# Optimization experiments

Measured on AMD Instinct MI355X. Metric: run time of the kernel, lower is better.

Reference implementation:

```python
import jax, jax.numpy as jnp
import numpy as np
import math

SEQ = 16384      # total ragged tokens
DIM = 1280       # vision hidden size
HEADS = 16
HDIM = DIM // HEADS  # 80
NSEG = 16        # number of segments (images); equal lengths of 1024


def rotate_half(x):
    x1, x2 = jnp.split(x, 2, axis=-1)
    return jnp.concatenate([-x2, x1], axis=-1)


def setup_inputs() -> dict:
    key = jax.random.key(0)
    ks = jax.random.split(key, 6)
    hidden_states = jax.random.normal(ks[0], (SEQ, DIM), dtype=jnp.float32)
    # rotary tables over the full head_dim (Qwen vision style: freqs duplicated)
    inv_freq = 1.0 / (10000.0 ** (jnp.arange(0, HDIM, 2, dtype=jnp.float32) / HDIM))
    pos = jnp.arange(SEQ, dtype=jnp.float32)
    freqs = jnp.outer(pos, inv_freq)                      # [S, HDIM/2]
    emb = jnp.concatenate([freqs, freqs], axis=-1)        # [S, HDIM]
    cos, sin = jnp.cos(emb), jnp.sin(emb)
    w_qkv = jax.random.normal(ks[1], (3 * DIM, DIM), dtype=jnp.float32) * 0.02
    b_qkv = jax.random.normal(ks[2], (3 * DIM,), dtype=jnp.float32) * 0.02
    w_proj = jax.random.normal(ks[3], (DIM, DIM), dtype=jnp.float32) * 0.02
    b_proj = jax.random.normal(ks[4], (DIM,), dtype=jnp.float32) * 0.02
    cu_seqlens = jnp.arange(NSEG + 1, dtype=jnp.int32) * (SEQ // NSEG)
    return {"hidden_states": hidden_states, "cos": cos, "sin": sin,
            "w_qkv": w_qkv, "b_qkv": b_qkv, "w_proj": w_proj, "b_proj": b_proj,
            "cu_seqlens": cu_seqlens}


def reference(hidden_states, cos, sin, w_qkv, b_qkv, w_proj, b_proj, cu_seqlens):
    S, D = hidden_states.shape
    hd = cos.shape[-1]
    nh = D // hd
    nseg = cu_seqlens.shape[0] - 1
    L = S // nseg  # equal segment lengths (matches cu_seqlens built in setup)

    qkv = hidden_states @ w_qkv.T + b_qkv                 # [S, 3D]
    qkv = qkv.reshape(S, 3, nh, hd)
    q, k, v = qkv[:, 0], qkv[:, 1], qkv[:, 2]             # [S, H, hd]

    # rotary (computed in float32, as in the original)
    c = cos[:, None, :]
    s = sin[:, None, :]
    q = q * c + rotate_half(q) * s
    k = k * c + rotate_half(k) * s

    # block-diagonal attention: reshape ragged-equal segments into a batch dim
    qs = q.reshape(nseg, L, nh, hd)
    ks = k.reshape(nseg, L, nh, hd)
    vs = v.reshape(nseg, L, nh, hd)

    scale = 1.0 / math.sqrt(hd)
    scores = jnp.einsum('bqhd,bkhd->bhqk', qs, ks) * scale   # [nseg, H, L, L]
    probs = jax.nn.softmax(scores, axis=-1)
    out = jnp.einsum('bhqk,bkhd->bqhd', probs, vs)           # [nseg, L, H, hd]
    out = out.reshape(S, D)
    return out @ w_proj.T + b_proj
```

## Files before the change

### kernel.cpp

```cpp
#include <hip/hip_runtime.h>

#define SEQ 16384
#define DIM 1280
#define NH 16
#define HD 80
#define NSEG 16
#define SEGL 1024

typedef __attribute__((ext_vector_type(8))) short bf16x8;
typedef __attribute__((ext_vector_type(4))) float f32x4;

__device__ inline unsigned short f2bf(float f){
  unsigned int x = __builtin_bit_cast(unsigned int, f);
  unsigned int r = (x + 0x7FFFu + ((x >> 16) & 1u)) >> 16;
  return (unsigned short)r;
}
__device__ inline float bf2f(unsigned short u){
  unsigned int x = ((unsigned int)u) << 16;
  return __builtin_bit_cast(float, x);
}
__device__ inline int cvtpk_bf16(float lo, float hi){
  int r;
  asm("v_cvt_pk_bf16_f32 %0, %1, %2" : "=v"(r) : "v"(lo), "v"(hi));
  return r;
}

__device__ inline void gload16(const unsigned short* g, unsigned short* l){
  __builtin_amdgcn_global_load_lds((const __attribute__((address_space(1))) void*)g,
                                   (__attribute__((address_space(3))) void*)l, 16, 0, 0);
}

__global__ __launch_bounds__(256) void pack3_kernel(const float* __restrict__ a,
    const float* __restrict__ b, const float* __restrict__ c,
    unsigned short* __restrict__ da, unsigned short* __restrict__ db,
    unsigned short* __restrict__ dc, int na, int nb){
  int i = blockIdx.x * 256 + threadIdx.x;
  const float* s; unsigned short* d; int j;
  if (i < na){ s = a; d = da; j = i; }
  else if (i < na + nb){ s = b; d = db; j = i - na; }
  else { s = c; d = dc; j = i - na - nb; }
  float4 v = ((const float4*)s)[j];
  ushort4 o;
  o.x = f2bf(v.x); o.y = f2bf(v.y); o.z = f2bf(v.z); o.w = f2bf(v.w);
  ((ushort4*)d)[j] = o;
}

template<int EPI>
__global__ __launch_bounds__(512, 2) void gemm256_kernel(const unsigned short* __restrict__ A,
    const unsigned short* __restrict__ B, const float* __restrict__ bias,
    void* __restrict__ Cout, unsigned short* __restrict__ Vtg, int M, int N, int K){
  __shared__ __attribute__((aligned(16))) unsigned short As[2][16384];
  __shared__ __attribute__((aligned(16))) unsigned short Bs[2][16384];
  const int nwg = gridDim.x;
  int bid = blockIdx.x;
  int swz = (bid & 7) * (nwg >> 3) + (bid >> 3);
  const int ntn = N >> 8;
  const int tm = (swz / ntn) << 8;
  const int tn = (swz % ntn) << 8;
  const int tid = threadIdx.x;
  const int wid = tid >> 6, l = tid & 63;
  const int lr = l & 15, lh = l >> 4;
  const int wrM = (wid >> 2) << 7;
  const int wcN = (wid & 3) << 6;
  const int NITER = K >> 7;

  const int srow = wid*8 + (l >> 3);
  const int scol = ((l & 7) ^ (l >> 3)) << 3;
  const int sldsu = wid << 9;

  const unsigned short* Ag = A + (size_t)tm * K;
  const unsigned short* Bg = B + (size_t)tn * K;

  const int ck0 = (lh*8) ^ ((l & 7) << 3);
  const int ck1 = (32 + lh*8) ^ ((l & 7) << 3);
  const int raA = (wrM + lr) << 6;
  const int raB = (wcN + lr) << 6;

  f32x4 zf = {0.f,0.f,0.f,0.f};
  f32x4 acc[8][4];
  #pragma unroll
  for (int i=0;i<8;i++)
    #pragma unroll
    for (int j=0;j<4;j++) acc[i][j] = zf;

#define STAGE_A(tile, h, q) gload16(Ag + (size_t)((h)*128 + (q)*64 + srow)*K + ((tile)<<6) + scol, \
                                    &As[(tile)&1][(h)*8192 + (q)*4096 + sldsu])
#define STAGE_B(tile, h, q) gload16(Bg + (size_t)((h)*128 + (q)*64 + srow)*K + ((tile)<<6) + scol, \
                                    &Bs[(tile)&1][(h)*8192 + (q)*4096 + sldsu])
#define RD_A(b, MOFF) \
  _Pragma("unroll") \
  for (int mi=0; mi<4; ++mi){ \
    a[0][mi] = *(const bf16x8*)&As[b][raA + ((MOFF)+mi)*1024 + ck0]; \
    a[1][mi] = *(const bf16x8*)&As[b][raA + ((MOFF)+mi)*1024 + ck1]; }
#define RD_B(b, NOFF, BREG) \
  _Pragma("unroll") \
  for (int nj=0; nj<2; ++nj){ \
    BREG[0][nj] = *(const bf16x8*)&Bs[b][raB + ((NOFF)+nj)*1024 + ck0]; \
    BREG[1][nj] = *(const bf16x8*)&Bs[b][raB + ((NOFF)+nj)*1024 + ck1]; }
#define BAR() __builtin_amdgcn_s_barrier();
#define QMFMA(MB, NB, BREG) \
  __builtin_amdgcn_s_setprio(1); \
  _Pragma("unroll") \
  for (int mi=0; mi<4; ++mi){ \
    _Pragma("unroll") \
    for (int nj=0; nj<2; ++nj){ \
      acc[(MB)+mi][(NB)+nj] = __builtin_amdgcn_mfma_f32_16x16x32_bf16(a[0][mi], BREG[0][nj], acc[(MB)+mi][(NB)+nj], 0,0,0); \
      acc[(MB)+mi][(NB)+nj] = __builtin_amdgcn_mfma_f32_16x16x32_bf16(a[1][mi], BREG[1][nj], acc[(MB)+mi][(NB)+nj], 0,0,0); \
    } \
  } \
  __builtin_amdgcn_s_setprio(0); \
  __builtin_amdgcn_s_barrier();

  #pragma unroll
  for (int q=0;q<2;q++){ STAGE_A(0,0,q); }
  #pragma unroll
  for (int q=0;q<2;q++){ STAGE_A(0,1,q); }
  #pragma unroll
  for (int q=0;q<2;q++){ STAGE_B(0,0,q); }
  #pragma unroll
  for (int q=0;q<2;q++){ STAGE_B(0,1,q); }
  #pragma unroll
  for (int q=0;q<2;q++){ STAGE_B(1,0,q); }
  #pragma unroll
  for (int q=0;q<2;q++){ STAGE_B(1,1,q); }
  #pragma unroll
  for (int q=0;q<2;q++){ STAGE_A(1,0,q); }
  #pragma unroll
  for (int q=0;q<2;q++){ STAGE_A(1,1,q); }
  asm volatile("s_waitcnt vmcnt(8)" ::: "memory");
  __builtin_amdgcn_s_barrier();

  for (int i=0; i<NITER; ++i){
    const int T = 2*i;
    const bool st = (i+1 < NITER);
    bf16x8 a[2][4], bx[2][2], by[2][2];

    RD_B(0, 0, bx); RD_A(0, 0);
    BAR(); QMFMA(0, 0, bx);

    RD_B(0, 2, by);
    BAR(); QMFMA(0, 2, by);

    RD_A(0, 4);
    if (st){ STAGE_B(T+2, 0, 0); STAGE_B(T+2, 0, 1); }
    BAR(); QMFMA(4, 2, by);

    if (st){
      STAGE_B(T+2, 1, 0); STAGE_B(T+2, 1, 1);
      STAGE_A(T+2, 0, 0); STAGE_A(T+2, 0, 1);
      asm volatile("s_waitcnt vmcnt(6)" ::: "memory");
    } else {
      asm volatile("s_waitcnt vmcnt(0)" ::: "memory");
    }
    BAR(); QMFMA(4, 0, bx);

    RD_B(1, 0, bx); RD_A(1, 0);
    if (st){ STAGE_A(T+2, 1, 0); STAGE_A(T+2, 1, 1); }
    BAR(); QMFMA(0, 0, bx);

    RD_B(1, 2, by);
    BAR(); QMFMA(0, 2, by);

    RD_A(1, 4);
    if (st){ STAGE_B(T+3, 0, 0); STAGE_B(T+3, 0, 1); STAGE_B(T+3, 1, 0); STAGE_B(T+3, 1, 1); }
    BAR(); QMFMA(4, 2, by);

    if (st){
      STAGE_A(T+3, 0, 0); STAGE_A(T+3, 0, 1); STAGE_A(T+3, 1, 0); STAGE_A(T+3, 1, 1);
      asm volatile("s_waitcnt vmcnt(8)" ::: "memory");
    }
    BAR(); QMFMA(4, 0, bx);
  }

#undef STAGE_A
#undef STAGE_B
#undef RD_A
#undef RD_B
#undef BAR
#undef QMFMA

  #pragma unroll
  for (int nj=0;nj<4;nj++){
    int col = tn + wcN + nj*16 + lr;
    float bv = bias[col];
    if (EPI == 0){
      int which = col / DIM;
      int rem = col - which*DIM;
      int hh = rem / HD;
      int d = rem - hh*HD;
      if (which == 2){
        unsigned short* Vd = Vtg + ((size_t)hh * HD + d) * SEQ;
        #pragma unroll
        for (int mi=0;mi<8;mi++){
          int row0 = tm + wrM + mi*16 + lh*4;
          int g = (row0 >> 2) & 15;
          int pg = ((g>>3)<<3) + ((g&3)<<1) + ((g>>2)&1);
          int s = (row0 & ~63) + pg*4;
          unsigned int w0 = (unsigned int)cvtpk_bf16(acc[mi][nj][0]+bv, acc[mi][nj][1]+bv);
          unsigned int w1 = (unsigned int)cvtpk_bf16(acc[mi][nj][2]+bv, acc[mi][nj][3]+bv);
          uint2 ov = {w0, w1};
          *(uint2*)(Vd + s) = ov;
        }
      } else {
        unsigned short* Q = (unsigned short*)Cout;
        size_t base = (size_t)(which*NH + hh) * SEQ;
        #pragma unroll
        for (int mi=0;mi<8;mi++){
          #pragma unroll
          for (int r=0;r<4;r++){
            int row = tm + wrM + mi*16 + lh*4 + r;
            Q[(base + row)*HD + d] = f2bf(acc[mi][nj][r] + bv);
          }
        }
      }
    } else {
      float* C = (float*)Cout;
      #pragma unroll
      for (int mi=0;mi<8;mi++){
        #pragma unroll
        for (int r=0;r<4;r++){
          int row = tm + wrM + mi*16 + lh*4 + r;
          C[(size_t)row*N + col] = acc[mi][nj][r] + bv;
        }
      }
    }
  }
}

__global__ __launch_bounds__(256) void rope_kernel(unsigned short* __restrict__ QKV,
    const float* __restrict__ cosb, const float* __restrict__ sinb){
  unsigned int gid = blockIdx.x * 256 + threadIdx.x;
  int pc = gid % 5;
  unsigned int row = gid / 5;
  int s = row % SEQ;
  int pd = pc * 8;
  float f = (row < (unsigned)(NH*SEQ)) ? (0.111803398874989485f * 1.4426950408889634f) : 1.0f;
  unsigned short* p = QKV + (size_t)row * HD;
  union { uint4 u4; unsigned short h[8]; } x1, x2, y1, y2;
  x1.u4 = *(const uint4*)(p + pd);
  x2.u4 = *(const uint4*)(p + pd + 40);
  float4 c0 = *(const float4*)(cosb + s*HD + pd);
  float4 c1 = *(const float4*)(cosb + s*HD + pd + 4);
  float4 s0 = *(const float4*)(sinb + s*HD + pd);
  float4 s1 = *(const float4*)(sinb + s*HD + pd + 4);
  float cc[8] = {c0.x,c0.y,c0.z,c0.w,c1.x,c1.y,c1.z,c1.w};
  float ss[8] = {s0.x,s0.y,s0.z,s0.w,s1.x,s1.y,s1.z,s1.w};
  #pragma unroll
  for (int j=0;j<8;j++){
    float a = bf2f(x1.h[j]), b = bf2f(x2.h[j]);
    y1.h[j] = f2bf((a*cc[j] - b*ss[j])*f);
    y2.h[j] = f2bf((b*cc[j] + a*ss[j])*f);
  }
  *(uint4*)(p + pd)      = y1.u4;
  *(uint4*)(p + pd + 40) = y2.u4;
}

__global__ __launch_bounds__(512) void attn_kernel(const unsigned short* __restrict__ QKV,
                                                   const unsigned short* __restrict__ Vt,
                                                   unsigned short* __restrict__ AO){
  int bid = blockIdx.x;
  int qt  = (bid >> 3) & 7;
  int g   = (bid & 7) * 32 + (bid >> 6);
  int h   = g & 15;
  int seg = g >> 4;
  int tid = threadIdx.x, wid = tid >> 6, l = tid & 63;
  int lr = l & 15, lh = l >> 4;
  const unsigned short* Qb = QKV + (size_t)(0*NH + h) * SEQ * HD;
  const unsigned short* Kb = QKV + (size_t)(1*NH + h) * SEQ * HD;
  const unsigned short* Vtb = Vt + (size_t)h * HD * SEQ;
  int q0 = seg*SEGL + qt*128;
  __shared__ __attribute__((aligned(16))) unsigned short Ksm[10240];
  __shared__ __attribute__((aligned(16))) unsigned short Vtsm[10240];
  bf16x8 qf[3];
  {
    const unsigned short* qp = Qb + (size_t)(q0 + wid*16 + lr) * HD;
    #pragma unroll
    for (int c=0;c<3;c++){
      int d0 = c*32 + lh*8;
      bf16x8 z = {0,0,0,0,0,0,0,0};
      qf[c] = (d0 < HD) ? *(const bf16x8*)(qp + d0) : z;
    }
  }
  f32x4 zf = {0.f,0.f,0.f,0.f};
  f32x4 o[5];
  #pragma unroll
  for (int dt=0;dt<5;dt++) o[dt] = zf;
  f32x4 lsumv = zf;
  float m = -1e30f;
  for (int kt=0; kt<8; kt++){
    int k0 = seg*SEGL + kt*128;
    const unsigned short* Ksrc = Kb + (size_t)k0 * HD;
    gload16(Ksrc + (wid*64 + l)*8,        &Ksm[wid*512]);
    gload16(Ksrc + (512 + wid*64 + l)*8,  &Ksm[4096 + wid*512]);
    if (wid < 4){
      gload16(Ksrc + (1024 + wid*64 + l)*8, &Ksm[8192 + wid*512]);
    } else {
      int cv = (wid-4)*64 + l;
      int d = cv >> 4, c16 = cv & 15;
      gload16(Vtb + (size_t)d*SEQ + k0 + ((c16 ^ (d & 15)) << 3), &Vtsm[(wid-4)*512]);
    }
    { int cv = 256 + wid*64 + l;
      int d = cv >> 4, c16 = cv & 15;
      gload16(Vtb + (size_t)d*SEQ + k0 + ((c16 ^ (d & 15)) << 3), &Vtsm[2048 + wid*512]); }
    { int cv = 768 + wid*64 + l;
      int d = cv >> 4, c16 = cv & 15;
      gload16(Vtb + (size_t)d*SEQ + k0 + ((c16 ^ (d & 15)) << 3), &Vtsm[6144 + wid*512]); }
    __syncthreads();
    f32x4 s[8];
    #pragma unroll
    for (int n=0;n<8;n++) s[n] = zf;
    #pragma unroll
    for (int c=0;c<3;c++){
      #pragma unroll
      for (int n=0;n<8;n++){
        bf16x8 kf = *(const bf16x8*)&Ksm[(n*16+lr)*80 + c*32 + lh*8];
        s[n] = __builtin_amdgcn_mfma_f32_16x16x32_bf16(kf, qf[c], s[n], 0,0,0);
      }
    }
    float pn[8];
    #pragma unroll
    for (int n=0;n<8;n++)
      pn[n] = fmaxf(fmaxf(s[n][0], s[n][1]), fmaxf(s[n][2], s[n][3]));
    float pm = fmaxf(fmaxf(fmaxf(pn[0],pn[1]), fmaxf(pn[2],pn[3])),
                     fmaxf(fmaxf(pn[4],pn[5]), fmaxf(pn[6],pn[7])));
    pm = fmaxf(pm, __shfl_xor(pm, 16));
    pm = fmaxf(pm, __shfl_xor(pm, 32));
    if (!__all(pm <= m + 8.f)){
      float mn = fmaxf(m, pm);
      float corr = exp2f(m - mn);
      #pragma unroll
      for (int r=0;r<4;r++) lsumv[r] *= corr;
      #pragma unroll
      for (int dt=0;dt<5;dt++)
        #pragma unroll
        for (int r=0;r<4;r++) o[dt][r] *= corr;
      m = mn;
    }
    #pragma unroll
    for (int n=0;n<8;n++)
      #pragma unroll
      for (int r=0;r<4;r++){
        float p = exp2f(s[n][r] - m);
        s[n][r] = p;
        lsumv[r] += p;
      }
    int w[16];
    #pragma unroll
    for (int n=0;n<8;n++){
      w[2*n]   = cvtpk_bf16(s[n][0], s[n][1]);
      w[2*n+1] = cvtpk_bf16(s[n][2], s[n][3]);
    }
    #pragma unroll
    for (int kc=0;kc<4;kc++){
      union { bf16x8 v; int u[4]; } pf;
      pf.u[0] = w[4*kc+0]; pf.u[1] = w[4*kc+1];
      pf.u[2] = w[4*kc+2]; pf.u[3] = w[4*kc+3];
      #pragma unroll
      for (int dt=0;dt<5;dt++){
        int row = dt*16 + lr;
        bf16x8 vf = *(const bf16x8*)&Vtsm[row*128 + ((kc*32 + lh*8) ^ ((row & 15) << 3))];
        o[dt] = __builtin_amdgcn_mfma_f32_16x16x32_bf16(vf, pf.v, o[dt], 0,0,0);
      }
    }
    __syncthreads();
  }
  float t = (lsumv[0] + lsumv[1]) + (lsumv[2] + lsumv[3]);
  t += __shfl_xor(t, 16);
  t += __shfl_xor(t, 32);
  float inv = 1.0f / t;
  int qrow = q0 + wid*16 + lr;
  unsigned short* op = AO + (size_t)qrow*DIM + h*HD;
  #pragma unroll
  for (int dt=0;dt<5;dt++){
    unsigned int w0 = (unsigned int)cvtpk_bf16(o[dt][0]*inv, o[dt][1]*inv);
    unsigned int w1 = (unsigned int)cvtpk_bf16(o[dt][2]*inv, o[dt][3]*inv);
    uint2 ov = {w0, w1};
    *(uint2*)(op + dt*16 + lh*4) = ov;
  }
}

extern "C" void kernel_launch(void* const* d_in, const int* in_sizes, int n_in,
                              void* d_out, int out_size, void* d_ws, size_t ws_size,
                              hipStream_t stream){
  const float* hs    = (const float*)d_in[0];
  const float* cosb  = (const float*)d_in[1];
  const float* sinb  = (const float*)d_in[2];
  const float* wqkv  = (const float*)d_in[3];
  const float* bqkv  = (const float*)d_in[4];
  const float* wproj = (const float*)d_in[5];
  const float* bproj = (const float*)d_in[6];
  float* out = (float*)d_out;

  unsigned short* Abf    = (unsigned short*)d_ws;
  unsigned short* Wqkvb  = Abf + (size_t)SEQ*DIM;
  unsigned short* Wprojb = Wqkvb + (size_t)3*DIM*DIM;
  unsigned short* QKVb   = Wprojb + (size_t)DIM*DIM;
  unsigned short* Vtb    = QKVb + (size_t)3*SEQ*DIM;
  unsigned short* AObf   = Abf;

  const int na = SEQ*DIM/4;
  const int nb = 3*DIM*DIM/4;
  const int nc = DIM*DIM/4;
  pack3_kernel<<<(na+nb+nc)/256, 256, 0, stream>>>(hs, wqkv, wproj, Abf, Wqkvb, Wprojb, na, nb);

  gemm256_kernel<0><<<(SEQ/256)*((3*DIM)/256), 512, 0, stream>>>(Abf, Wqkvb, bqkv,
                                                                 (void*)QKVb, Vtb, SEQ, 3*DIM, DIM);

  rope_kernel<<<(2*NH*SEQ*5)/256, 256, 0, stream>>>(QKVb, cosb, sinb);

  attn_kernel<<<NSEG*NH*(SEGL/128), 512, 0, stream>>>(QKVb, Vtb, AObf);

  gemm256_kernel<1><<<(SEQ/256)*(DIM/256), 512, 0, stream>>>(AObf, Wprojb, bproj,
                                                             (void*)out, nullptr, SEQ, DIM, DIM);
}
```

Measured before the change: 447.6 us.

## Make GEMM kernel persistent and prefetch next tile during last K-step

Both GEMMs now launch a fixed 256-workgroup grid, and each workgroup loops over output tiles with a grid-stride. During the final K iteration of a tile it issues the global-to-LDS loads for the first two K slices of its next tile, so that tile's prologue overlaps the current epilogue. The aim is to remove per-block launch and prologue latency and keep the memory pipeline busy across tile boundaries. In exchange, registers must be held across the loop and the code gets more complex. Load balance is unchanged for the QKV GEMM (960 tiles over 256 blocks).

Result: slower. 481.4 us (+7.5%).

```diff
diff --git a/kernel.cpp b/kernel.cpp
--- a/kernel.cpp
+++ b/kernel.cpp
@@ -51,25 +51,18 @@
     void* __restrict__ Cout, unsigned short* __restrict__ Vtg, int M, int N, int K){
   __shared__ __attribute__((aligned(16))) unsigned short As[2][16384];
   __shared__ __attribute__((aligned(16))) unsigned short Bs[2][16384];
-  const int nwg = gridDim.x;
-  int bid = blockIdx.x;
-  int swz = (bid & 7) * (nwg >> 3) + (bid >> 3);
   const int ntn = N >> 8;
-  const int tm = (swz / ntn) << 8;
-  const int tn = (swz % ntn) << 8;
+  const int ntiles = (M >> 8) * ntn;
+  const int NITER = K >> 7;
   const int tid = threadIdx.x;
   const int wid = tid >> 6, l = tid & 63;
   const int lr = l & 15, lh = l >> 4;
   const int wrM = (wid >> 2) << 7;
   const int wcN = (wid & 3) << 6;
-  const int NITER = K >> 7;
 
   const int srow = wid*8 + (l >> 3);
   const int scol = ((l & 7) ^ (l >> 3)) << 3;
   const int sldsu = wid << 9;
-
-  const unsigned short* Ag = A + (size_t)tm * K;
-  const unsigned short* Bg = B + (size_t)tn * K;
 
   const int ck0 = (lh*8) ^ ((l & 7) << 3);
   const int ck1 = (32 + lh*8) ^ ((l & 7) << 3);
@@ -77,16 +70,11 @@
   const int raB = (wcN + lr) << 6;
 
   f32x4 zf = {0.f,0.f,0.f,0.f};
-  f32x4 acc[8][4];
-  #pragma unroll
-  for (int i=0;i<8;i++)
-    #pragma unroll
-    for (int j=0;j<4;j++) acc[i][j] = zf;
-
-#define STAGE_A(tile, h, q) gload16(Ag + (size_t)((h)*128 + (q)*64 + srow)*K + ((tile)<<6) + scol, \
-                                    &As[(tile)&1][(h)*8192 + (q)*4096 + sldsu])
-#define STAGE_B(tile, h, q) gload16(Bg + (size_t)((h)*128 + (q)*64 + srow)*K + ((tile)<<6) + scol, \
-                                    &Bs[(tile)&1][(h)*8192 + (q)*4096 + sldsu])
+
+#define STG_A(base, col, buf, h, q) gload16((base) + (size_t)((h)*128 + (q)*64 + srow)*K + (col) + scol, \
+                                            &As[buf][(h)*8192 + (q)*4096 + sldsu])
+#define STG_B(base, col, buf, h, q) gload16((base) + (size_t)((h)*128 + (q)*64 + srow)*K + (col) + scol, \
+                                            &Bs[buf][(h)*8192 + (q)*4096 + sldsu])
 #define RD_A(b, MOFF) \
   _Pragma("unroll") \
   for (int mi=0; mi<4; ++mi){ \
@@ -111,120 +99,191 @@
   __builtin_amdgcn_s_setprio(0); \
   __builtin_amdgcn_s_barrier();
 
-  #pragma unroll
-  for (int q=0;q<2;q++){ STAGE_A(0,0,q); }
-  #pragma unroll
-  for (int q=0;q<2;q++){ STAGE_A(0,1,q); }
-  #pragma unroll
-  for (int q=0;q<2;q++){ STAGE_B(0,0,q); }
-  #pragma unroll
-  for (int q=0;q<2;q++){ STAGE_B(0,1,q); }
-  #pragma unroll
-  for (int q=0;q<2;q++){ STAGE_B(1,0,q); }
-  #pragma unroll
-  for (int q=0;q<2;q++){ STAGE_B(1,1,q); }
-  #pragma unroll
-  for (int q=0;q<2;q++){ STAGE_A(1,0,q); }
-  #pragma unroll
-  for (int q=0;q<2;q++){ STAGE_A(1,1,q); }
+  int tix = blockIdx.x;
+  int swz = (tix & 7) * (ntiles >> 3) + (tix >> 3);
+  int tm = (swz / ntn) << 8;
+  int tn = (swz % ntn) << 8;
+  const unsigned short* Ag = A + (size_t)tm * K;
+  const unsigned short* Bg = B + (size_t)tn * K;
+
+  #pragma unroll
+  for (int q=0;q<2;q++){ STG_A(Ag, 0, 0, 0, q); }
+  #pragma unroll
+  for (int q=0;q<2;q++){ STG_A(Ag, 0, 0, 1, q); }
+  #pragma unroll
+  for (int q=0;q<2;q++){ STG_B(Bg, 0, 0, 0, q); }
+  #pragma unroll
+  for (int q=0;q<2;q++){ STG_B(Bg, 0, 0, 1, q); }
+  #pragma unroll
+  for (int q=0;q<2;q++){ STG_B(Bg, 64, 1, 0, q); }
+  #pragma unroll
+  for (int q=0;q<2;q++){ STG_B(Bg, 64, 1, 1, q); }
+  #pragma unroll
+  for (int q=0;q<2;q++){ STG_A(Ag, 64, 1, 0, q); }
+  #pragma unroll
+  for (int q=0;q<2;q++){ STG_A(Ag, 64, 1, 1, q); }
   asm volatile("s_waitcnt vmcnt(8)" ::: "memory");
   __builtin_amdgcn_s_barrier();
 
-  for (int i=0; i<NITER; ++i){
-    const int T = 2*i;
-    const bool st = (i+1 < NITER);
-    bf16x8 a[2][4], bx[2][2], by[2][2];
-
-    RD_B(0, 0, bx); RD_A(0, 0);
-    BAR(); QMFMA(0, 0, bx);
-
-    RD_B(0, 2, by);
-    BAR(); QMFMA(0, 2, by);
-
-    RD_A(0, 4);
-    if (st){ STAGE_B(T+2, 0, 0); STAGE_B(T+2, 0, 1); }
-    BAR(); QMFMA(4, 2, by);
-
-    if (st){
-      STAGE_B(T+2, 1, 0); STAGE_B(T+2, 1, 1);
-      STAGE_A(T+2, 0, 0); STAGE_A(T+2, 0, 1);
+  while (true){
+    const bool hn = (tix + (int)gridDim.x) < ntiles;
+    int tm2 = 0, tn2 = 0;
+    const unsigned short* Agn = Ag;
+    const unsigned short* Bgn = Bg;
+    if (hn){
+      int tix2 = tix + gridDim.x;
+      int swz2 = (tix2 & 7) * (ntiles >> 3) + (tix2 >> 3);
+      tm2 = (swz2 / ntn) << 8;
+      tn2 = (swz2 % ntn) << 8;
+      Agn = A + (size_t)tm2 * K;
+      Bgn = B + (size_t)tn2 * K;
+    }
+
+    f32x4 acc[8][4];
+    #pragma unroll
+    for (int i=0;i<8;i++)
+      #pragma unroll
+      for (int j=0;j<4;j++) acc[i][j] = zf;
+
+    for (int i=0; i<NITER-1; ++i){
+      const int T = 2*i;
+      bf16x8 a[2][4], bx[2][2], by[2][2];
+
+      RD_B(0, 0, bx); RD_A(0, 0);
+      BAR(); QMFMA(0, 0, bx);
+
+      RD_B(0, 2, by);
+      BAR(); QMFMA(0, 2, by);
+
+      RD_A(0, 4);
+      STG_B(Bg, (T+2)<<6, 0, 0, 0); STG_B(Bg, (T+2)<<6, 0, 0, 1);
+      BAR(); QMFMA(4, 2, by);
+
+      STG_B(Bg, (T+2)<<6, 0, 1, 0); STG_B(Bg, (T+2)<<6, 0, 1, 1);
+      STG_A(Ag, (T+2)<<6, 0, 0, 0); STG_A(Ag, (T+2)<<6, 0, 0, 1);
       asm volatile("s_waitcnt vmcnt(6)" ::: "memory");
-    } else {
-      asm volatile("s_waitcnt vmcnt(0)" ::: "memory");
-    }
-    BAR(); QMFMA(4, 0, bx);
-
-    RD_B(1, 0, bx); RD_A(1, 0);
-    if (st){ STAGE_A(T+2, 1, 0); STAGE_A(T+2, 1, 1); }
-    BAR(); QMFMA(0, 0, bx);
-
-    RD_B(1, 2, by);
-    BAR(); QMFMA(0, 2, by);
-
-    RD_A(1, 4);
-    if (st){ STAGE_B(T+3, 0, 0); STAGE_B(T+3, 0, 1); STAGE_B(T+3, 1, 0); STAGE_B(T+3, 1, 1); }
-    BAR(); QMFMA(4, 2, by);
-
-    if (st){
-      STAGE_A(T+3, 0, 0); STAGE_A(T+3, 0, 1); STAGE_A(T+3, 1, 0); STAGE_A(T+3, 1, 1);
+      BAR(); QMFMA(4, 0, bx);
+
+      RD_B(1, 0, bx); RD_A(1, 0);
+      STG_A(Ag, (T+2)<<6, 0, 1, 0); STG_A(Ag, (T+2)<<6, 0, 1, 1);
+      BAR(); QMFMA(0, 0, bx);
+
+      RD_B(1, 2, by);
+      BAR(); QMFMA(0, 2, by);
+
+      RD_A(1, 4);
+      STG_B(Bg, (T+3)<<6, 1, 0, 0); STG_B(Bg, (T+3)<<6, 1, 0, 1);
+      STG_B(Bg, (T+3)<<6, 1, 1, 0); STG_B(Bg, (T+3)<<6, 1, 1, 1);
+      BAR(); QMFMA(4, 2, by);
+
+      STG_A(Ag, (T+3)<<6, 1, 0, 0); STG_A(Ag, (T+3)<<6, 1, 0, 1);
+      STG_A(Ag, (T+3)<<6, 1, 1, 0); STG_A(Ag, (T+3)<<6, 1, 1, 1);
       asm volatile("s_waitcnt vmcnt(8)" ::: "memory");
-    }
-    BAR(); QMFMA(4, 0, bx);
-  }
-
-#undef STAGE_A
-#undef STAGE_B
-#undef RD_A
-#undef RD_B
-#undef BAR
-#undef QMFMA
-
-  #pragma unroll
-  for (int nj=0;nj<4;nj++){
-    int col = tn + wcN + nj*16 + lr;
-    float bv = bias[col];
-    if (EPI == 0){
-      int which = col / DIM;
-      int rem = col - which*DIM;
-      int hh = rem / HD;
-      int d = rem - hh*HD;
-      if (which == 2){
-        unsigned short* Vd = Vtg + ((size_t)hh * HD + d) * SEQ;
-        #pragma unroll
-        for (int mi=0;mi<8;mi++){
-          int row0 = tm + wrM + mi*16 + lh*4;
-          int g = (row0 >> 2) & 15;
-          int pg = ((g>>3)<<3) + ((g&3)<<1) + ((g>>2)&1);
-          int s = (row0 & ~63) + pg*4;
-          unsigned int w0 = (unsigned int)cvtpk_bf16(acc[mi][nj][0]+bv, acc[mi][nj][1]+bv);
-          unsigned int w1 = (unsigned int)cvtpk_bf16(acc[mi][nj][2]+bv, acc[mi][nj][3]+bv);
-          uint2 ov = {w0, w1};
-          *(uint2*)(Vd + s) = ov;
+      BAR(); QMFMA(4, 0, bx);
+    }
+
+    {
+      bf16x8 a[2][4], bx[2][2], by[2][2];
+
+      RD_B(0, 0, bx); RD_A(0, 0);
+      BAR(); QMFMA(0, 0, bx);
+
+      RD_B(0, 2, by);
+      BAR(); QMFMA(0, 2, by);
+
+      RD_A(0, 4);
+      if (hn){ STG_B(Bgn, 0, 0, 0, 0); STG_B(Bgn, 0, 0, 0, 1); }
+      BAR(); QMFMA(4, 2, by);
+
+      if (hn){
+        STG_B(Bgn, 0, 0, 1, 0); STG_B(Bgn, 0, 0, 1, 1);
+        STG_A(Agn, 0, 0, 0, 0); STG_A(Agn, 0, 0, 0, 1);
+        asm volatile("s_waitcnt vmcnt(6)" ::: "memory");
+      } else {
+        asm volatile("s_waitcnt vmcnt(0)" ::: "memory");
+      }
+      BAR(); QMFMA(4, 0, bx);
+
+      RD_B(1, 0, bx); RD_A(1, 0);
+      if (hn){ STG_A(Agn, 0, 0, 1, 0); STG_A(Agn, 0, 0, 1, 1); }
+      BAR(); QMFMA(0, 0, bx);
+
+      RD_B(1, 2, by);
+      BAR(); QMFMA(0, 2, by);
+
+      RD_A(1, 4);
+      if (hn){
+        STG_B(Bgn, 64, 1, 0, 0); STG_B(Bgn, 64, 1, 0, 1);
+        STG_B(Bgn, 64, 1, 1, 0); STG_B(Bgn, 64, 1, 1, 1);
+      }
+      BAR(); QMFMA(4, 2, by);
+
+      if (hn){
+        STG_A(Agn, 64, 1, 0, 0); STG_A(Agn, 64, 1, 0, 1);
+        STG_A(Agn, 64, 1, 1, 0); STG_A(Agn, 64, 1, 1, 1);
+        asm volatile("s_waitcnt vmcnt(8)" ::: "memory");
+      }
+      BAR(); QMFMA(4, 0, bx);
+    }
+
+    #pragma unroll
+    for (int nj=0;nj<4;nj++){
+      int col = tn + wcN + nj*16 + lr;
+      float bv = bias[col];
+      if (EPI == 0){
+        int which = col / DIM;
+        int rem = col - which*DIM;
+        int hh = rem / HD;
+        int d = rem - hh*HD;
+        if (which == 2){
+          unsigned short* Vd = Vtg + ((size_t)hh * HD + d) * SEQ;
+          #pragma unroll
+          for (int mi=0;mi<8;mi++){
+            int row0 = tm + wrM + mi*16 + lh*4;
+            int g = (row0 >> 2) & 15;
+            int pg = ((g>>3)<<3) + ((g&3)<<1) + ((g>>2)&1);
+            int s = (row0 & ~63) + pg*4;
+            unsigned int w0 = (unsigned int)cvtpk_bf16(acc[mi][nj][0]+bv, acc[mi][nj][1]+bv);
+            unsigned int w1 = (unsigned int)cvtpk_bf16(acc[mi][nj][2]+bv, acc[mi][nj][3]+bv);
+            uint2 ov = {w0, w1};
+            *(uint2*)(Vd + s) = ov;
+          }
+        } else {
+          unsigned short* Q = (unsigned short*)Cout;
+          size_t base = (size_t)(which*NH + hh) * SEQ;
+          #pragma unroll
+          for (int mi=0;mi<8;mi++){
+            #pragma unroll
+            for (int r=0;r<4;r++){
+              int row = tm + wrM + mi*16 + lh*4 + r;
+              Q[(base + row)*HD + d] = f2bf(acc[mi][nj][r] + bv);
+            }
+          }
         }
       } else {
-        unsigned short* Q = (unsigned short*)Cout;
-        size_t base = (size_t)(which*NH + hh) * SEQ;
+        float* C = (float*)Cout;
         #pragma unroll
         for (int mi=0;mi<8;mi++){
           #pragma unroll
           for (int r=0;r<4;r++){
             int row = tm + wrM + mi*16 + lh*4 + r;
-            Q[(base + row)*HD + d] = f2bf(acc[mi][nj][r] + bv);
+            C[(size_t)row*N + col] = acc[mi][nj][r] + bv;
           }
         }
       }
-    } else {
-      float* C = (float*)Cout;
-      #pragma unroll
-      for (int mi=0;mi<8;mi++){
-        #pragma unroll
-        for (int r=0;r<4;r++){
-          int row = tm + wrM + mi*16 + lh*4 + r;
-          C[(size_t)row*N + col] = acc[mi][nj][r] + bv;
-        }
-      }
-    }
+    }
+
+    if (!hn) break;
+    tix += gridDim.x;
+    tm = tm2; tn = tn2; Ag = Agn; Bg = Bgn;
   }
+
+#undef STG_A
+#undef STG_B
+#undef RD_A
+#undef RD_B
+#undef BAR
+#undef QMFMA
 }
 
 __global__ __launch_bounds__(256) void rope_kernel(unsigned short* __restrict__ QKV,
@@ -403,13 +462,13 @@
   const int nc = DIM*DIM/4;
   pack3_kernel<<<(na+nb+nc)/256, 256, 0, stream>>>(hs, wqkv, wproj, Abf, Wqkvb, Wprojb, na, nb);
 
-  gemm256_kernel<0><<<(SEQ/256)*((3*DIM)/256), 512, 0, stream>>>(Abf, Wqkvb, bqkv,
-                                                                 (void*)QKVb, Vtb, SEQ, 3*DIM, DIM);
+  gemm256_kernel<0><<<256, 512, 0, stream>>>(Abf, Wqkvb, bqkv,
+                                             (void*)QKVb, Vtb, SEQ, 3*DIM, DIM);
 
   rope_kernel<<<(2*NH*SEQ*5)/256, 256, 0, stream>>>(QKVb, cosb, sinb);
 
   attn_kernel<<<NSEG*NH*(SEGL/128), 512, 0, stream>>>(QKVb, Vtb, AObf);
 
-  gemm256_kernel<1><<<(SEQ/256)*(DIM/256), 512, 0, stream>>>(AObf, Wprojb, bproj,
-                                                             (void*)out, nullptr, SEQ, DIM, DIM);
-}
+  gemm256_kernel<1><<<256, 512, 0, stream>>>(AObf, Wprojb, bproj,
+                                             (void*)out, nullptr, SEQ, DIM, DIM);
+}
```

## Process two 16-row query tiles per wave in attention with 256-thread blocks

Applied to the files above, without the earlier changes.

The attention kernel now runs 4 waves per block instead of 8, and each wave handles 32 query rows as two 16-row subtiles (A and B). Each K and V fragment read from LDS is reused for two MFMAs, halving LDS read traffic per unit of compute, and each thread issues five K and five V global-to-LDS loads per tile instead of about three. The cost is roughly twice the accumulator and score registers per wave, which may lower occupancy, and fewer waves per block to hide load latency.

Measured after the change: 459.7 us. +2.7%, slower.

```diff
diff --git a/kernel.cpp b/kernel.cpp
--- a/kernel.cpp
+++ b/kernel.cpp
@@ -255,7 +255,7 @@
   *(uint4*)(p + pd + 40) = y2.u4;
 }
 
-__global__ __launch_bounds__(512) void attn_kernel(const unsigned short* __restrict__ QKV,
+__global__ __launch_bounds__(256) void attn_kernel(const unsigned short* __restrict__ QKV,
                                                    const unsigned short* __restrict__ Vt,
                                                    unsigned short* __restrict__ AO){
   int bid = blockIdx.x;
@@ -271,111 +271,164 @@
   int q0 = seg*SEGL + qt*128;
   __shared__ __attribute__((aligned(16))) unsigned short Ksm[10240];
   __shared__ __attribute__((aligned(16))) unsigned short Vtsm[10240];
-  bf16x8 qf[3];
+  bf16x8 qfA[3], qfB[3];
   {
-    const unsigned short* qp = Qb + (size_t)(q0 + wid*16 + lr) * HD;
+    const unsigned short* qpA = Qb + (size_t)(q0 + wid*32 + lr) * HD;
+    const unsigned short* qpB = qpA + (size_t)16 * HD;
     #pragma unroll
     for (int c=0;c<3;c++){
       int d0 = c*32 + lh*8;
       bf16x8 z = {0,0,0,0,0,0,0,0};
-      qf[c] = (d0 < HD) ? *(const bf16x8*)(qp + d0) : z;
+      qfA[c] = (d0 < HD) ? *(const bf16x8*)(qpA + d0) : z;
+      qfB[c] = (d0 < HD) ? *(const bf16x8*)(qpB + d0) : z;
     }
   }
   f32x4 zf = {0.f,0.f,0.f,0.f};
-  f32x4 o[5];
-  #pragma unroll
-  for (int dt=0;dt<5;dt++) o[dt] = zf;
-  f32x4 lsumv = zf;
-  float m = -1e30f;
+  f32x4 oA[5], oB[5];
+  #pragma unroll
+  for (int dt=0;dt<5;dt++){ oA[dt] = zf; oB[dt] = zf; }
+  f32x4 lsA = zf, lsB = zf;
+  float mA = -1e30f, mB = -1e30f;
   for (int kt=0; kt<8; kt++){
     int k0 = seg*SEGL + kt*128;
     const unsigned short* Ksrc = Kb + (size_t)k0 * HD;
-    gload16(Ksrc + (wid*64 + l)*8,        &Ksm[wid*512]);
-    gload16(Ksrc + (512 + wid*64 + l)*8,  &Ksm[4096 + wid*512]);
-    if (wid < 4){
-      gload16(Ksrc + (1024 + wid*64 + l)*8, &Ksm[8192 + wid*512]);
-    } else {
-      int cv = (wid-4)*64 + l;
+    #pragma unroll
+    for (int r=0;r<5;r++)
+      gload16(Ksrc + (size_t)(r*256 + wid*64 + l)*8, &Ksm[r*2048 + wid*512]);
+    #pragma unroll
+    for (int r=0;r<5;r++){
+      int cv = r*256 + wid*64 + l;
       int d = cv >> 4, c16 = cv & 15;
-      gload16(Vtb + (size_t)d*SEQ + k0 + ((c16 ^ (d & 15)) << 3), &Vtsm[(wid-4)*512]);
-    }
-    { int cv = 256 + wid*64 + l;
-      int d = cv >> 4, c16 = cv & 15;
-      gload16(Vtb + (size_t)d*SEQ + k0 + ((c16 ^ (d & 15)) << 3), &Vtsm[2048 + wid*512]); }
-    { int cv = 768 + wid*64 + l;
-      int d = cv >> 4, c16 = cv & 15;
-      gload16(Vtb + (size_t)d*SEQ + k0 + ((c16 ^ (d & 15)) << 3), &Vtsm[6144 + wid*512]); }
+      gload16(Vtb + (size_t)d*SEQ + k0 + ((c16 ^ (d & 15)) << 3), &Vtsm[r*2048 + wid*512]);
+    }
     __syncthreads();
-    f32x4 s[8];
-    #pragma unroll
-    for (int n=0;n<8;n++) s[n] = zf;
+    f32x4 sA[8], sB[8];
+    #pragma unroll
+    for (int n=0;n<8;n++){ sA[n] = zf; sB[n] = zf; }
     #pragma unroll
     for (int c=0;c<3;c++){
       #pragma unroll
       for (int n=0;n<8;n++){
         bf16x8 kf = *(const bf16x8*)&Ksm[(n*16+lr)*80 + c*32 + lh*8];
-        s[n] = __builtin_amdgcn_mfma_f32_16x16x32_bf16(kf, qf[c], s[n], 0,0,0);
-      }
-    }
-    float pn[8];
-    #pragma unroll
-    for (int n=0;n<8;n++)
-      pn[n] = fmaxf(fmaxf(s[n][0], s[n][1]), fmaxf(s[n][2], s[n][3]));
-    float pm = fmaxf(fmaxf(fmaxf(pn[0],pn[1]), fmaxf(pn[2],pn[3])),
-                     fmaxf(fmaxf(pn[4],pn[5]), fmaxf(pn[6],pn[7])));
-    pm = fmaxf(pm, __shfl_xor(pm, 16));
-    pm = fmaxf(pm, __shfl_xor(pm, 32));
-    if (!__all(pm <= m + 8.f)){
-      float mn = fmaxf(m, pm);
-      float corr = exp2f(m - mn);
-      #pragma unroll
-      for (int r=0;r<4;r++) lsumv[r] *= corr;
-      #pragma unroll
-      for (int dt=0;dt<5;dt++)
-        #pragma unroll
-        for (int r=0;r<4;r++) o[dt][r] *= corr;
-      m = mn;
-    }
-    #pragma unroll
-    for (int n=0;n<8;n++)
-      #pragma unroll
-      for (int r=0;r<4;r++){
-        float p = exp2f(s[n][r] - m);
-        s[n][r] = p;
-        lsumv[r] += p;
-      }
-    int w[16];
-    #pragma unroll
-    for (int n=0;n<8;n++){
-      w[2*n]   = cvtpk_bf16(s[n][0], s[n][1]);
-      w[2*n+1] = cvtpk_bf16(s[n][2], s[n][3]);
+        sA[n] = __builtin_amdgcn_mfma_f32_16x16x32_bf16(kf, qfA[c], sA[n], 0,0,0);
+        sB[n] = __builtin_amdgcn_mfma_f32_16x16x32_bf16(kf, qfB[c], sB[n], 0,0,0);
+      }
+    }
+    int wA[16], wB[16];
+    {
+      float pn[8];
+      #pragma unroll
+      for (int n=0;n<8;n++)
+        pn[n] = fmaxf(fmaxf(sA[n][0], sA[n][1]), fmaxf(sA[n][2], sA[n][3]));
+      float pm = fmaxf(fmaxf(fmaxf(pn[0],pn[1]), fmaxf(pn[2],pn[3])),
+                       fmaxf(fmaxf(pn[4],pn[5]), fmaxf(pn[6],pn[7])));
+      pm = fmaxf(pm, __shfl_xor(pm, 16));
+      pm = fmaxf(pm, __shfl_xor(pm, 32));
+      if (!__all(pm <= mA + 8.f)){
+        float mn = fmaxf(mA, pm);
+        float corr = exp2f(mA - mn);
+        #pragma unroll
+        for (int r=0;r<4;r++) lsA[r] *= corr;
+        #pragma unroll
+        for (int dt=0;dt<5;dt++)
+          #pragma unroll
+          for (int r=0;r<4;r++) oA[dt][r] *= corr;
+        mA = mn;
+      }
+      #pragma unroll
+      for (int n=0;n<8;n++)
+        #pragma unroll
+        for (int r=0;r<4;r++){
+          float p = exp2f(sA[n][r] - mA);
+          sA[n][r] = p;
+          lsA[r] += p;
+        }
+      #pragma unroll
+      for (int n=0;n<8;n++){
+        wA[2*n]   = cvtpk_bf16(sA[n][0], sA[n][1]);
+        wA[2*n+1] = cvtpk_bf16(sA[n][2], sA[n][3]);
+      }
+    }
+    {
+      float pn[8];
+      #pragma unroll
+      for (int n=0;n<8;n++)
+        pn[n] = fmaxf(fmaxf(sB[n][0], sB[n][1]), fmaxf(sB[n][2], sB[n][3]));
+      float pm = fmaxf(fmaxf(fmaxf(pn[0],pn[1]), fmaxf(pn[2],pn[3])),
+                       fmaxf(fmaxf(pn[4],pn[5]), fmaxf(pn[6],pn[7])));
+      pm = fmaxf(pm, __shfl_xor(pm, 16));
+      pm = fmaxf(pm, __shfl_xor(pm, 32));
+      if (!__all(pm <= mB + 8.f)){
+        float mn = fmaxf(mB, pm);
+        float corr = exp2f(mB - mn);
+        #pragma unroll
+        for (int r=0;r<4;r++) lsB[r] *= corr;
+        #pragma unroll
+        for (int dt=0;dt<5;dt++)
+          #pragma unroll
+          for (int r=0;r<4;r++) oB[dt][r] *= corr;
+        mB = mn;
+      }
+      #pragma unroll
+      for (int n=0;n<8;n++)
+        #pragma unroll
+        for (int r=0;r<4;r++){
+          float p = exp2f(sB[n][r] - mB);
+          sB[n][r] = p;
+          lsB[r] += p;
+        }
+      #pragma unroll
+      for (int n=0;n<8;n++){
+        wB[2*n]   = cvtpk_bf16(sB[n][0], sB[n][1]);
+        wB[2*n+1] = cvtpk_bf16(sB[n][2], sB[n][3]);
+      }
     }
     #pragma unroll
     for (int kc=0;kc<4;kc++){
-      union { bf16x8 v; int u[4]; } pf;
-      pf.u[0] = w[4*kc+0]; pf.u[1] = w[4*kc+1];
-      pf.u[2] = w[4*kc+2]; pf.u[3] = w[4*kc+3];
+      union { bf16x8 v; int u[4]; } pfA, pfB;
+      pfA.u[0] = wA[4*kc+0]; pfA.u[1] = wA[4*kc+1];
+      pfA.u[2] = wA[4*kc+2]; pfA.u[3] = wA[4*kc+3];
+      pfB.u[0] = wB[4*kc+0]; pfB.u[1] = wB[4*kc+1];
+      pfB.u[2] = wB[4*kc+2]; pfB.u[3] = wB[4*kc+3];
       #pragma unroll
       for (int dt=0;dt<5;dt++){
         int row = dt*16 + lr;
         bf16x8 vf = *(const bf16x8*)&Vtsm[row*128 + ((kc*32 + lh*8) ^ ((row & 15) << 3))];
-        o[dt] = __builtin_amdgcn_mfma_f32_16x16x32_bf16(vf, pf.v, o[dt], 0,0,0);
+        oA[dt] = __builtin_amdgcn_mfma_f32_16x16x32_bf16(vf, pfA.v, oA[dt], 0,0,0);
+        oB[dt] = __builtin_amdgcn_mfma_f32_16x16x32_bf16(vf, pfB.v, oB[dt], 0,0,0);
       }
     }
     __syncthreads();
   }
-  float t = (lsumv[0] + lsumv[1]) + (lsumv[2] + lsumv[3]);
-  t += __shfl_xor(t, 16);
-  t += __shfl_xor(t, 32);
-  float inv = 1.0f / t;
-  int qrow = q0 + wid*16 + lr;
-  unsigned short* op = AO + (size_t)qrow*DIM + h*HD;
-  #pragma unroll
-  for (int dt=0;dt<5;dt++){
-    unsigned int w0 = (unsigned int)cvtpk_bf16(o[dt][0]*inv, o[dt][1]*inv);
-    unsigned int w1 = (unsigned int)cvtpk_bf16(o[dt][2]*inv, o[dt][3]*inv);
-    uint2 ov = {w0, w1};
-    *(uint2*)(op + dt*16 + lh*4) = ov;
+  {
+    float t = (lsA[0] + lsA[1]) + (lsA[2] + lsA[3]);
+    t += __shfl_xor(t, 16);
+    t += __shfl_xor(t, 32);
+    float inv = 1.0f / t;
+    int qrow = q0 + wid*32 + lr;
+    unsigned short* op = AO + (size_t)qrow*DIM + h*HD;
+    #pragma unroll
+    for (int dt=0;dt<5;dt++){
+      unsigned int w0 = (unsigned int)cvtpk_bf16(oA[dt][0]*inv, oA[dt][1]*inv);
+      unsigned int w1 = (unsigned int)cvtpk_bf16(oA[dt][2]*inv, oA[dt][3]*inv);
+      uint2 ov = {w0, w1};
+      *(uint2*)(op + dt*16 + lh*4) = ov;
+    }
+  }
+  {
+    float t = (lsB[0] + lsB[1]) + (lsB[2] + lsB[3]);
+    t += __shfl_xor(t, 16);
+    t += __shfl_xor(t, 32);
+    float inv = 1.0f / t;
+    int qrow = q0 + wid*32 + 16 + lr;
+    unsigned short* op = AO + (size_t)qrow*DIM + h*HD;
+    #pragma unroll
+    for (int dt=0;dt<5;dt++){
+      unsigned int w0 = (unsigned int)cvtpk_bf16(oB[dt][0]*inv, oB[dt][1]*inv);
+      unsigned int w1 = (unsigned int)cvtpk_bf16(oB[dt][2]*inv, oB[dt][3]*inv);
+      uint2 ov = {w0, w1};
+      *(uint2*)(op + dt*16 + lh*4) = ov;
+    }
   }
 }
 
@@ -408,7 +461,7 @@
 
   rope_kernel<<<(2*NH*SEQ*5)/256, 256, 0, stream>>>(QKVb, cosb, sinb);
 
-  attn_kernel<<<NSEG*NH*(SEGL/128), 512, 0, stream>>>(QKVb, Vtb, AObf);
+  attn_kernel<<<NSEG*NH*(SEGL/128), 256, 0, stream>>>(QKVb, Vtb, AObf);
 
   gemm256_kernel<1><<<(SEQ/256)*(DIM/256), 512, 0, stream>>>(AObf, Wprojb, bproj,
                                                              (void*)out, nullptr, SEQ, DIM, DIM);
```
